# Kernel tuning notes

Hardware: AMD Instinct MI355X
Metric: run time of the kernel (lower is better)

## Reference

```python
import jax, jax.numpy as jnp
import numpy as np

B, S, E, P = 4, 2048, 1024, 4096

def setup_inputs() -> dict:
    key = jax.random.key(0)
    kx, kk, kv = jax.random.split(key, 3)
    x = jax.random.normal(kx, (B, S, E), dtype=jnp.float32)
    K = jax.random.normal(kk, (P, E), dtype=jnp.float32)
    V = jax.random.normal(kv, (P, E), dtype=jnp.float32)
    return {"x": x, "K": K, "V": V}

def reference(x, K, V):
    # scores: [B, S, P] = x @ K^T scaled by 1/sqrt(E)
    scale = jnp.asarray(x.shape[-1], x.dtype) ** -0.5
    scores = jnp.einsum('bse,pe->bsp', x, K) * scale
    attn = jax.nn.softmax(scores, axis=-1)
    # output: [B, S, E] = attn @ V
    return jnp.einsum('bsp,pe->bse', attn, V)
```

## Files before the change

kernel.cpp:

```cpp
#include <hip/hip_runtime.h>
#include <hip/hip_bf16.h>

typedef __attribute__((ext_vector_type(8))) short bf16x8;
typedef __attribute__((ext_vector_type(4))) float f32x4;
typedef __attribute__((ext_vector_type(8))) unsigned short u16x8;

__device__ __forceinline__ unsigned short f2bf(float f) {
  union { float f; unsigned u; } c; c.f = f;
  unsigned u = c.u;
  u = (u + 0x7FFFu + ((u >> 16) & 1u)) >> 16;
  return (unsigned short)u;
}

__device__ __forceinline__ void gld_lds16(const void* g, void* l) {
  __builtin_amdgcn_global_load_lds(
      (__attribute__((address_space(1))) unsigned int*)g,
      (__attribute__((address_space(3))) unsigned int*)l,
      16, 0, 0);
}

__global__ void cvt_all(const float* __restrict__ x, unsigned short* __restrict__ x16,
                        const float* __restrict__ Kw, unsigned short* __restrict__ K16,
                        const float* __restrict__ V, unsigned short* __restrict__ Vt,
                        float* __restrict__ lsum) {
  const int b = blockIdx.x;
  if (b < 32) lsum[b * 256 + threadIdx.x] = 0.f;

  if (b < 6144) {
    const float* in;
    unsigned short* out;
    int i;
    if (b < 4096) {
      in = x; out = x16; i = (b * 256 + threadIdx.x) * 8;
    } else {
      in = Kw; out = K16; i = ((b - 4096) * 256 + threadIdx.x) * 8;
    }
    const float4* p = (const float4*)(in + i);
    float4 a = p[0], bb = p[1];
    u16x8 r;
    r[0] = f2bf(a.x); r[1] = f2bf(a.y); r[2] = f2bf(a.z); r[3] = f2bf(a.w);
    r[4] = f2bf(bb.x); r[5] = f2bf(bb.y); r[6] = f2bf(bb.z); r[7] = f2bf(bb.w);
    *(u16x8*)(out + i) = r;
  } else {
    __shared__ unsigned short t[64][65];
    const int tile = b - 6144;
    const int p0 = (tile & 63) * 64;
    const int e0 = (tile >> 6) * 64;
    const int tx = threadIdx.x & 63;
    const int ty = threadIdx.x >> 6;
#pragma unroll
    for (int i = 0; i < 16; ++i) {
      int p = ty + i * 4;
      t[p][tx] = f2bf(V[(size_t)(p0 + p) * 1024 + e0 + tx]);
    }
    __syncthreads();
#pragma unroll
    for (int i = 0; i < 16; ++i) {
      int e = ty + i * 4;
      Vt[(size_t)(e0 + e) * 4096 + p0 + tx] = t[tx][e];
    }
  }
}

template <int EPI>
__global__ __launch_bounds__(512, 2) void gemm8p(
    const unsigned short* __restrict__ A, const unsigned short* __restrict__ B,
    unsigned short* __restrict__ Pout, float* __restrict__ lsum,
    float* __restrict__ Cout, const float* __restrict__ lin, float scale) {
  constexpr int BM = EPI ? 128 : 256;
  constexpr int BN = 256;
  constexpr int Kd = EPI ? 4096 : 1024;
  constexpr int Nc = EPI ? 1024 : 4096;
  constexpr int NT = Kd / 64;
  constexpr int AU = BM / 128;
  constexpr int NU = AU + 2;
  constexpr int M_rep = BM / 32;
  constexpr int PH = M_rep / 2;

  __shared__ __align__(16) char lds[2 * NU * 16384];

  const int tid = threadIdx.x;
  const int lane = tid & 63;
  const int w = tid >> 6;
  const int wm = w >> 2;
  const int wn = w & 3;
  const int q = lane >> 4;
  const int ml = lane & 15;

  const int bid = blockIdx.x;
  const int wg = (bid & 7) * (EPI ? 32 : 64) + (bid >> 3);
  const int m_t = EPI ? (wg >> 2) : (wg >> 4);
  const int n_t = EPI ? (wg & 3) : (wg & 15);
  const int row0 = m_t * BM;
  const int col0 = n_t * BN;

  const int cr = tid >> 3;
  const int ss = (tid & 7) ^ (cr & 7);
  char* ldsw = lds + w * 1024 + lane * 16;

  const int ccB = (q ^ (ml & 7)) * 16;
  const int aOff = (EPI ? 0 : wm) * 16384 + ((EPI ? wm * 64 : 0) + ml) * 128 + ccB;
  const int bOff = (AU + (wn >> 1)) * 16384 + ((wn & 1) * 64 + ml) * 128 + ccB;

  f32x4 acc[M_rep][4] = {};
  bf16x8 bF[4][2];

  auto stA = [&](int a, int t, int buf) {
    const unsigned short* s = A + (size_t)(row0 + a * 128 + cr) * Kd + t * 64 + ss * 8;
    char* d = ldsw + (buf * NU + a) * 16384;
    gld_lds16(s, d);
    gld_lds16(s + (size_t)64 * Kd, d + 8192);
  };
  auto stB = [&](int b, int t, int buf) {
    const unsigned short* s = B + (size_t)(col0 + b * 128 + cr) * Kd + t * 64 + ss * 8;
    char* d = ldsw + (buf * NU + AU + b) * 16384;
    gld_lds16(s, d);
    gld_lds16(s + (size_t)64 * Kd, d + 8192);
  };

#pragma unroll
  for (int a = 0; a < AU; ++a) stA(a, 0, 0);
  stB(0, 0, 0); stB(1, 0, 0);
  stB(0, 1, 1); stB(1, 1, 1);
  asm volatile("s_waitcnt vmcnt(4)" ::: "memory");
  __builtin_amdgcn_s_barrier();

#pragma unroll 2
  for (int g = 0; g < NT; ++g) {
    const char* base = lds + (g & 1) * (NU * 16384);
    const int tA = (g + 1) & (NT - 1);
    const int bufA = (g + 1) & 1;
    const int tB = (g + 2) & (NT - 1);
    const int bufB = g & 1;
#pragma unroll
    for (int p = 0; p < PH; ++p) {
      if (p == 0) {
#pragma unroll
        for (int ni = 0; ni < 4; ++ni)
#pragma unroll
          for (int ks = 0; ks < 2; ++ks)
            bF[ni][ks] = *(const bf16x8*)(base + ((bOff ^ (ks * 64)) + ni * 2048));
      }
      bf16x8 aF[2][2];
#pragma unroll
      for (int i = 0; i < 2; ++i)
#pragma unroll
        for (int ks = 0; ks < 2; ++ks)
          aF[i][ks] = *(const bf16x8*)(base + ((aOff ^ (ks * 64)) + (2 * p + i) * 2048));

      if constexpr (EPI == 0) {
        if (p == 0) stA(0, tA, bufA);
        else if (p == 1) stA(1, tA, bufA);
        else if (p == 2) stB(0, tB, bufB);
        else stB(1, tB, bufB);
      } else {
        if (p == 0) stA(0, tA, bufA);
        else { stB(0, tB, bufB); stB(1, tB, bufB); }
      }

      __builtin_amdgcn_s_barrier();
      asm volatile("s_waitcnt lgkmcnt(0)" ::: "memory");
      __builtin_amdgcn_sched_barrier(0);
      __builtin_amdgcn_s_setprio(1);
#pragma unroll
      for (int ks = 0; ks < 2; ++ks)
#pragma unroll
        for (int i = 0; i < 2; ++i)
#pragma unroll
          for (int ni = 0; ni < 4; ++ni)
            acc[2 * p + i][ni] = __builtin_amdgcn_mfma_f32_16x16x32_bf16(
                aF[i][ks], bF[ni][ks], acc[2 * p + i][ni], 0, 0, 0);
      __builtin_amdgcn_s_setprio(0);
      if (p == PH - 1) asm volatile("s_waitcnt vmcnt(4)" ::: "memory");
      __builtin_amdgcn_s_barrier();
    }
  }

  if constexpr (EPI == 0) {
#pragma unroll
    for (int mi = 0; mi < M_rep; ++mi) {
#pragma unroll
      for (int j = 0; j < 4; ++j) {
        const int gr = row0 + wm * (BM / 2) + mi * 16 + q * 4 + j;
        float rsum = 0.f;
#pragma unroll
        for (int ni = 0; ni < 4; ++ni) {
          const int gc = col0 + wn * 64 + ni * 16 + ml;
          float pv = exp2f(acc[mi][ni][j] * scale);
          rsum += pv;
          Pout[(size_t)gr * Nc + gc] = f2bf(pv);
        }
        rsum += __shfl_xor(rsum, 1);
        rsum += __shfl_xor(rsum, 2);
        rsum += __shfl_xor(rsum, 4);
        rsum += __shfl_xor(rsum, 8);
        if (ml == 0) atomicAdd(&lsum[gr], rsum);
      }
    }
  } else {
#pragma unroll
    for (int mi = 0; mi < M_rep; ++mi) {
#pragma unroll
      for (int j = 0; j < 4; ++j) {
        const int gr = row0 + wm * (BM / 2) + mi * 16 + q * 4 + j;
        const float rl = 1.0f / lin[gr];
#pragma unroll
        for (int ni = 0; ni < 4; ++ni) {
          const int gc = col0 + wn * 64 + ni * 16 + ml;
          Cout[(size_t)gr * Nc + gc] = acc[mi][ni][j] * rl;
        }
      }
    }
  }
}

extern "C" void kernel_launch(void* const* d_in, const int* in_sizes, int n_in,
                              void* d_out, int out_size, void* d_ws,
                              size_t ws_size, hipStream_t stream) {
  const float* x = (const float*)d_in[0];
  const float* Kw = (const float*)d_in[1];
  const float* Vw = (const float*)d_in[2];
  float* out = (float*)d_out;
  char* ws = (char*)d_ws;

  unsigned short* x16  = (unsigned short*)(ws);
  unsigned short* K16  = (unsigned short*)(ws + (16u << 20));
  unsigned short* V16t = (unsigned short*)(ws + (24u << 20));
  float*          lsum = (float*)(ws + (32u << 20));
  unsigned short* P16  = (unsigned short*)(ws + (33u << 20));

  cvt_all<<<7168, 256, 0, stream>>>(x, x16, Kw, K16, Vw, V16t, lsum);

  gemm8p<0><<<512, 512, 0, stream>>>(
      x16, K16, P16, lsum, nullptr, nullptr,
      0.03125f * 1.44269504088896340736f);
  gemm8p<1><<<256, 512, 0, stream>>>(
      P16, V16t, nullptr, nullptr, out, lsum, 0.f);
}
```

Before: 255.7 us.

## Double-buffer A fragments across MFMA phases and vectorize V transpose stores

The GEMM main loop is restructured so the A-fragment LDS reads for the next phase, including the first phase of the next K tile, are issued before the current phase's MFMAs. A partial lgkmcnt wait replaces the full drain, so LDS reads can overlap matrix math. The V transpose in the conversion kernel now writes 8 bf16 values per thread as one 16-byte store instead of scalar 2-byte stores. The cost is more live registers and hand-tuned waitcnt and barrier ordering that must stay correct across both epilogue variants.

After: 251.1 us. No clear change (-1.8%).

```diff
diff --git a/kernel.cpp b/kernel.cpp
--- a/kernel.cpp
+++ b/kernel.cpp
@@ -24,16 +24,17 @@
                         const float* __restrict__ V, unsigned short* __restrict__ Vt,
                         float* __restrict__ lsum) {
   const int b = blockIdx.x;
-  if (b < 32) lsum[b * 256 + threadIdx.x] = 0.f;
+  const int tid = threadIdx.x;
+  if (b < 32) lsum[b * 256 + tid] = 0.f;
 
   if (b < 6144) {
     const float* in;
     unsigned short* out;
     int i;
     if (b < 4096) {
-      in = x; out = x16; i = (b * 256 + threadIdx.x) * 8;
+      in = x; out = x16; i = (b * 256 + tid) * 8;
     } else {
-      in = Kw; out = K16; i = ((b - 4096) * 256 + threadIdx.x) * 8;
+      in = Kw; out = K16; i = ((b - 4096) * 256 + tid) * 8;
     }
     const float4* p = (const float4*)(in + i);
     float4 a = p[0], bb = p[1];
@@ -46,18 +47,23 @@
     const int tile = b - 6144;
     const int p0 = (tile & 63) * 64;
     const int e0 = (tile >> 6) * 64;
-    const int tx = threadIdx.x & 63;
-    const int ty = threadIdx.x >> 6;
+    const int tx = tid & 63;
+    const int ty = tid >> 6;
 #pragma unroll
     for (int i = 0; i < 16; ++i) {
       int p = ty + i * 4;
       t[p][tx] = f2bf(V[(size_t)(p0 + p) * 1024 + e0 + tx]);
     }
     __syncthreads();
-#pragma unroll
-    for (int i = 0; i < 16; ++i) {
-      int e = ty + i * 4;
-      Vt[(size_t)(e0 + e) * 4096 + p0 + tx] = t[tx][e];
+    const int op = (tid & 7) * 8;
+    const int oe = tid >> 3;
+#pragma unroll
+    for (int h = 0; h < 2; ++h) {
+      int e = oe + h * 32;
+      u16x8 r;
+#pragma unroll
+      for (int i = 0; i < 8; ++i) r[i] = t[op + i][e];
+      *(u16x8*)(Vt + (size_t)(e0 + e) * 4096 + p0 + op) = r;
     }
   }
 }
@@ -68,14 +74,12 @@
     unsigned short* __restrict__ Pout, float* __restrict__ lsum,
     float* __restrict__ Cout, const float* __restrict__ lin, float scale) {
   constexpr int BM = EPI ? 128 : 256;
-  constexpr int BN = 256;
   constexpr int Kd = EPI ? 4096 : 1024;
   constexpr int Nc = EPI ? 1024 : 4096;
   constexpr int NT = Kd / 64;
   constexpr int AU = BM / 128;
   constexpr int NU = AU + 2;
   constexpr int M_rep = BM / 32;
-  constexpr int PH = M_rep / 2;
 
   __shared__ __align__(16) char lds[2 * NU * 16384];
 
@@ -92,11 +96,11 @@
   const int m_t = EPI ? (wg >> 2) : (wg >> 4);
   const int n_t = EPI ? (wg & 3) : (wg & 15);
   const int row0 = m_t * BM;
-  const int col0 = n_t * BN;
+  const int col0 = n_t * 256;
 
   const int cr = tid >> 3;
   const int ss = (tid & 7) ^ (cr & 7);
-  char* ldsw = lds + w * 1024 + lane * 16;
+  char* ldsw = lds + w * 1024;
 
   const int ccB = (q ^ (ml & 7)) * 16;
   const int aOff = (EPI ? 0 : wm) * 16384 + ((EPI ? wm * 64 : 0) + ml) * 128 + ccB;
@@ -104,6 +108,7 @@
 
   f32x4 acc[M_rep][4] = {};
   bf16x8 bF[4][2];
+  bf16x8 aF[2][2][2];
 
   auto stA = [&](int a, int t, int buf) {
     const unsigned short* s = A + (size_t)(row0 + a * 128 + cr) * Kd + t * 64 + ss * 8;
@@ -118,60 +123,106 @@
     gld_lds16(s + (size_t)64 * Kd, d + 8192);
   };
 
+  auto ldA = [&](int par, const char* bs, int ph) {
+#pragma unroll
+    for (int i = 0; i < 2; ++i)
+#pragma unroll
+      for (int ks = 0; ks < 2; ++ks)
+        aF[par][i][ks] = *(const bf16x8*)(bs + (aOff ^ (ks * 64)) + (2 * ph + i) * 2048);
+  };
+  auto mf = [&](int p, bf16x8 (&af)[2][2]) {
+#pragma unroll
+    for (int ks = 0; ks < 2; ++ks)
+#pragma unroll
+      for (int i = 0; i < 2; ++i)
+#pragma unroll
+        for (int ni = 0; ni < 4; ++ni)
+          acc[2 * p + i][ni] = __builtin_amdgcn_mfma_f32_16x16x32_bf16(
+              af[i][ks], bF[ni][ks], acc[2 * p + i][ni], 0, 0, 0);
+  };
+
 #pragma unroll
   for (int a = 0; a < AU; ++a) stA(a, 0, 0);
   stB(0, 0, 0); stB(1, 0, 0);
   stB(0, 1, 1); stB(1, 1, 1);
   asm volatile("s_waitcnt vmcnt(4)" ::: "memory");
   __builtin_amdgcn_s_barrier();
+  __builtin_amdgcn_sched_barrier(0);
+  ldA(0, lds, 0);
 
 #pragma unroll 2
   for (int g = 0; g < NT; ++g) {
     const char* base = lds + (g & 1) * (NU * 16384);
+    const char* baseN = lds + ((g + 1) & 1) * (NU * 16384);
     const int tA = (g + 1) & (NT - 1);
     const int bufA = (g + 1) & 1;
     const int tB = (g + 2) & (NT - 1);
     const int bufB = g & 1;
-#pragma unroll
-    for (int p = 0; p < PH; ++p) {
-      if (p == 0) {
-#pragma unroll
-        for (int ni = 0; ni < 4; ++ni)
-#pragma unroll
-          for (int ks = 0; ks < 2; ++ks)
-            bF[ni][ks] = *(const bf16x8*)(base + ((bOff ^ (ks * 64)) + ni * 2048));
-      }
-      bf16x8 aF[2][2];
-#pragma unroll
-      for (int i = 0; i < 2; ++i)
-#pragma unroll
-        for (int ks = 0; ks < 2; ++ks)
-          aF[i][ks] = *(const bf16x8*)(base + ((aOff ^ (ks * 64)) + (2 * p + i) * 2048));
-
-      if constexpr (EPI == 0) {
-        if (p == 0) stA(0, tA, bufA);
-        else if (p == 1) stA(1, tA, bufA);
-        else if (p == 2) stB(0, tB, bufB);
-        else stB(1, tB, bufB);
-      } else {
-        if (p == 0) stA(0, tA, bufA);
-        else { stB(0, tB, bufB); stB(1, tB, bufB); }
-      }
-
-      __builtin_amdgcn_s_barrier();
-      asm volatile("s_waitcnt lgkmcnt(0)" ::: "memory");
-      __builtin_amdgcn_sched_barrier(0);
-      __builtin_amdgcn_s_setprio(1);
+
+#pragma unroll
+    for (int ni = 0; ni < 4; ++ni)
 #pragma unroll
       for (int ks = 0; ks < 2; ++ks)
-#pragma unroll
-        for (int i = 0; i < 2; ++i)
-#pragma unroll
-          for (int ni = 0; ni < 4; ++ni)
-            acc[2 * p + i][ni] = __builtin_amdgcn_mfma_f32_16x16x32_bf16(
-                aF[i][ks], bF[ni][ks], acc[2 * p + i][ni], 0, 0, 0);
-      __builtin_amdgcn_s_setprio(0);
-      if (p == PH - 1) asm volatile("s_waitcnt vmcnt(4)" ::: "memory");
+        bF[ni][ks] = *(const bf16x8*)(base + (bOff ^ (ks * 64)) + ni * 2048);
+    __builtin_amdgcn_sched_barrier(0);
+    ldA(1, base, 1);
+    stA(0, tA, bufA);
+    if constexpr (EPI == 0) stA(1, tA, bufA);
+    __builtin_amdgcn_sched_barrier(0);
+    __builtin_amdgcn_s_barrier();
+    asm volatile("s_waitcnt lgkmcnt(4)" ::: "memory");
+    __builtin_amdgcn_sched_barrier(0);
+    __builtin_amdgcn_s_setprio(1);
+    mf(0, aF[0]);
+    __builtin_amdgcn_s_setprio(0);
+    __builtin_amdgcn_s_barrier();
+
+    if constexpr (EPI == 0) {
+      ldA(0, base, 2);
+      stB(0, tB, bufB);
+      __builtin_amdgcn_sched_barrier(0);
+      __builtin_amdgcn_s_barrier();
+      asm volatile("s_waitcnt lgkmcnt(4)" ::: "memory");
+      __builtin_amdgcn_sched_barrier(0);
+      __builtin_amdgcn_s_setprio(1);
+      mf(1, aF[1]);
+      __builtin_amdgcn_s_setprio(0);
+      __builtin_amdgcn_s_barrier();
+
+      ldA(1, base, 3);
+      stB(1, tB, bufB);
+      __builtin_amdgcn_sched_barrier(0);
+      __builtin_amdgcn_s_barrier();
+      asm volatile("s_waitcnt lgkmcnt(4)" ::: "memory");
+      __builtin_amdgcn_sched_barrier(0);
+      __builtin_amdgcn_s_setprio(1);
+      mf(2, aF[0]);
+      __builtin_amdgcn_s_setprio(0);
+      asm volatile("s_waitcnt vmcnt(4)" ::: "memory");
+      __builtin_amdgcn_s_barrier();
+      __builtin_amdgcn_sched_barrier(0);
+
+      ldA(0, baseN, 0);
+      __builtin_amdgcn_sched_barrier(0);
+      __builtin_amdgcn_s_barrier();
+      asm volatile("s_waitcnt lgkmcnt(4)" ::: "memory");
+      __builtin_amdgcn_sched_barrier(0);
+      __builtin_amdgcn_s_setprio(1);
+      mf(3, aF[1]);
+      __builtin_amdgcn_s_setprio(0);
+      __builtin_amdgcn_s_barrier();
+    } else {
+      stB(0, tB, bufB);
+      stB(1, tB, bufB);
+      asm volatile("s_waitcnt vmcnt(4)" ::: "memory");
+      __builtin_amdgcn_s_barrier();
+      __builtin_amdgcn_sched_barrier(0);
+      ldA(0, baseN, 0);
+      asm volatile("s_waitcnt lgkmcnt(4)" ::: "memory");
+      __builtin_amdgcn_sched_barrier(0);
+      __builtin_amdgcn_s_setprio(1);
+      mf(1, aF[1]);
+      __builtin_amdgcn_s_setprio(0);
       __builtin_amdgcn_s_barrier();
     }
   }
```
